# Optimization experiments

Measured on AMD Instinct MI355X. Metric: run time of the kernel, lower is better.

## Reference

```python
import jax, jax.numpy as jnp
import numpy as np

INV_SQRT2 = 0.7071067811865476  # Haar (db1) lowpass on a length-1 zero-padded signal: cA = x/sqrt(2)


def setup_inputs() -> dict:
    key = jax.random.key(0)
    k = jax.random.split(key, 6)
    batch, node, dim = 4, 512, 64
    x = jax.random.normal(k[0], (batch, node, dim), dtype=jnp.float32)
    w0 = jax.random.normal(k[1], (1, 1), dtype=jnp.float32)   # linear[0].weight (always index 0 in source)
    b0 = jax.random.normal(k[2], (1,), dtype=jnp.float32)     # linear[0].bias
    wa = jax.random.normal(k[3], (dim,), dtype=jnp.float32)   # stacked attn_fc[i].weight (each 1x1)
    ba = jax.random.normal(k[4], (dim,), dtype=jnp.float32)   # stacked attn_fc[i].bias
    adj = jax.random.randint(k[5], (node, node), 0, 2, dtype=jnp.int32)
    return {"x": x, "w0": w0, "b0": b0, "wa": wa, "ba": ba, "adj": adj}


def reference(x, w0, b0, wa, ba, adj):
    # x: (b, n, d). Per-channel wavelet feature: softplus(linear0(cA)), cA = x/sqrt(2).
    feat = jax.nn.softplus(x * (INV_SQRT2 * w0[0, 0]) + b0[0])          # (b, n, d)
    scores = feat * wa + ba                                              # (b, n, d): attn_fc[i] per channel
    mask = adj > 0                                                       # (n, n)
    # attn_matrix[b,i,j,d] = scores[b,j,d] * mask[i,j], then masked-fill -1e9 where mask==0
    logits = scores[:, None, :, :] * mask[None, :, :, None].astype(scores.dtype)
    logits = jnp.where(mask[None, :, :, None], logits, jnp.float32(-1e9))
    attn = jax.nn.softmax(logits, axis=2)                                # softmax over j (neighbors)
    out = jnp.einsum('bijd,bjd->bid', attn, feat)                        # (b, n, d)
    return out
```

## Files before the change

kernel.cpp:

```cpp
#include <hip/hip_runtime.h>

#define NODE 512
#define DIM 64
#define BATCH 4

typedef __attribute__((ext_vector_type(8))) short bf16x8;
typedef __attribute__((ext_vector_type(4))) float f32x4;

__device__ __forceinline__ unsigned short f2bf(float f) {
    unsigned int u = __float_as_uint(f);
    u += 0x7FFF + ((u >> 16) & 1);
    return (unsigned short)(u >> 16);
}

__global__ __launch_bounds__(256) void k_fused(const float* __restrict__ x,
                                               const float* __restrict__ w0,
                                               const float* __restrict__ b0,
                                               const float* __restrict__ wa,
                                               const float* __restrict__ ba,
                                               const int* __restrict__ adj,
                                               float* __restrict__ out) {
    const int blk = blockIdx.x;
    const int dt = blk & 3;
    const int it = (blk >> 2) & 31;
    const int b  = blk >> 7;
    const int lane = threadIdx.x & 63;
    const int w    = threadIdx.x >> 6;
    const int fr = lane & 15;
    const int kg = lane >> 4;
    const int i0 = it * 16;
    const int d  = dt * 16 + fr;

    const float c   = 0.7071067811865476f * w0[0];
    const float bb  = b0[0];
    const float wad = wa[d], bad = ba[d];

    const int k0 = w * 128 + kg * 8;
    const int*   pAdj = adj + (i0 + fr) * NODE + k0;
    const float* px   = x + (size_t)b * NODE * DIM + d;

    f32x4 accD = {0.f, 0.f, 0.f, 0.f};
    f32x4 accN = {0.f, 0.f, 0.f, 0.f};

    #pragma unroll
    for (int m = 0; m < 4; ++m) {
        const int jb = k0 + m * 32;
        int4 a0 = *(const int4*)(pAdj + m * 32);
        int4 a1 = *(const int4*)(pAdj + m * 32 + 4);
        union { bf16x8 v; unsigned short s[8]; } A, BD, BN;
        A.s[0] = a0.x ? 0x3F80 : 0;  A.s[1] = a0.y ? 0x3F80 : 0;
        A.s[2] = a0.z ? 0x3F80 : 0;  A.s[3] = a0.w ? 0x3F80 : 0;
        A.s[4] = a1.x ? 0x3F80 : 0;  A.s[5] = a1.y ? 0x3F80 : 0;
        A.s[6] = a1.z ? 0x3F80 : 0;  A.s[7] = a1.w ? 0x3F80 : 0;
        #pragma unroll
        for (int t = 0; t < 8; ++t) {
            float xx = px[(size_t)(jb + t) * DIM];
            float z  = fmaf(xx, c, bb);
            float f  = fmaxf(z, 0.f) + __logf(1.f + __expf(-fabsf(z)));
            float e  = __expf(fmaf(f, wad, bad));
            BD.s[t] = f2bf(e);
            BN.s[t] = f2bf(e * f);
        }
        accD = __builtin_amdgcn_mfma_f32_16x16x32_bf16(A.v, BD.v, accD, 0, 0, 0);
        accN = __builtin_amdgcn_mfma_f32_16x16x32_bf16(A.v, BN.v, accN, 0, 0, 0);
    }

    __shared__ f32x4 red[2][4][64];
    red[0][w][lane] = accD;
    red[1][w][lane] = accN;
    __syncthreads();

    if (w == 0) {
        f32x4 D = red[0][0][lane] + red[0][1][lane] + red[0][2][lane] + red[0][3][lane];
        f32x4 N = red[1][0][lane] + red[1][1][lane] + red[1][2][lane] + red[1][3][lane];
        #pragma unroll
        for (int r = 0; r < 4; ++r) {
            float dd = D[r], nn = N[r];
            float o = (dd != 0.f) ? nn / dd : 0.f;
            out[((b * NODE) + i0 + kg * 4 + r) * DIM + dt * 16 + fr] = o;
        }
    }
}

extern "C" void kernel_launch(void* const* d_in, const int* in_sizes, int n_in,
                              void* d_out, int out_size, void* d_ws, size_t ws_size,
                              hipStream_t stream) {
    const float* x  = (const float*)d_in[0];
    const float* w0 = (const float*)d_in[1];
    const float* b0 = (const float*)d_in[2];
    const float* wa = (const float*)d_in[3];
    const float* ba = (const float*)d_in[4];
    const int*  adj = (const int*)d_in[5];
    float* out = (float*)d_out;

    k_fused<<<dim3(BATCH * 32 * 4), dim3(256), 0, stream>>>(
        x, w0, b0, wa, ba, adj, out);
}
```

Before: 10.56 us.

## Precompute softplus/exp features into LDS and share across two row tiles

Each block now computes the per-neighbor transcendental features (e and e*f in bf16) for all 512 nodes and its 16 channels once, using coalesced float4 loads, and stores them in shared memory. Eight waves then run the MFMA masked sums for two 16-row tiles that read B operands from LDS. Previously every wave recomputed these features per row tile with strided scalar loads. The cost is a larger block, about 33KB of LDS and an extra barrier, and the grid shrinks from 512 to 256 blocks.

Result: faster. 10.32 us (-2.2%).

```diff
diff --git a/kernel.cpp b/kernel.cpp
--- a/kernel.cpp
+++ b/kernel.cpp
@@ -7,77 +7,97 @@
 typedef __attribute__((ext_vector_type(8))) short bf16x8;
 typedef __attribute__((ext_vector_type(4))) float f32x4;
 
+#define LSTRIDE 520
+
 __device__ __forceinline__ unsigned short f2bf(float f) {
     unsigned int u = __float_as_uint(f);
     u += 0x7FFF + ((u >> 16) & 1);
     return (unsigned short)(u >> 16);
 }
 
-__global__ __launch_bounds__(256) void k_fused(const float* __restrict__ x,
-                                               const float* __restrict__ w0,
-                                               const float* __restrict__ b0,
-                                               const float* __restrict__ wa,
-                                               const float* __restrict__ ba,
-                                               const int* __restrict__ adj,
-                                               float* __restrict__ out) {
+__global__ __launch_bounds__(512) void k_fused2(const float* __restrict__ x,
+                                                const float* __restrict__ w0,
+                                                const float* __restrict__ b0,
+                                                const float* __restrict__ wa,
+                                                const float* __restrict__ ba,
+                                                const int* __restrict__ adj,
+                                                float* __restrict__ out) {
+    __shared__ unsigned short Ep[16][LSTRIDE];
+    __shared__ unsigned short Wp[16][LSTRIDE];
+    __shared__ f32x4 red[2][4][2][64];
+
     const int blk = blockIdx.x;
-    const int dt = blk & 3;
-    const int it = (blk >> 2) & 31;
-    const int b  = blk >> 7;
-    const int lane = threadIdx.x & 63;
-    const int w    = threadIdx.x >> 6;
+    const int dt  = blk & 3;
+    const int itg = (blk >> 2) & 15;
+    const int b   = blk >> 6;
+    const int tid = threadIdx.x;
+    const int i0  = itg * 32;
+    const int d0  = dt * 16;
+
+    {
+        const float c  = 0.7071067811865476f * w0[0];
+        const float bb = b0[0];
+        #pragma unroll
+        for (int iter = 0; iter < 4; ++iter) {
+            const int task = iter * 512 + tid;
+            const int dg = task & 3;
+            const int j  = task >> 2;
+            const float4 xx = *(const float4*)(x + ((size_t)(b * NODE + j) * DIM) + d0 + dg * 4);
+            #pragma unroll
+            for (int i = 0; i < 4; ++i) {
+                const int dl = dg * 4 + i;
+                const float xv = (i == 0) ? xx.x : (i == 1) ? xx.y : (i == 2) ? xx.z : xx.w;
+                float z = fmaf(xv, c, bb);
+                float f = fmaxf(z, 0.f) + __logf(1.f + __expf(-fabsf(z)));
+                float e = __expf(fmaf(f, wa[d0 + dl], ba[d0 + dl]));
+                Ep[dl][j] = f2bf(e);
+                Wp[dl][j] = f2bf(e * f);
+            }
+        }
+    }
+    __syncthreads();
+
+    const int lane = tid & 63;
+    const int w    = tid >> 6;
+    const int itl  = w & 1;
+    const int kq   = w >> 1;
     const int fr = lane & 15;
     const int kg = lane >> 4;
-    const int i0 = it * 16;
-    const int d  = dt * 16 + fr;
 
-    const float c   = 0.7071067811865476f * w0[0];
-    const float bb  = b0[0];
-    const float wad = wa[d], bad = ba[d];
-
-    const int k0 = w * 128 + kg * 8;
-    const int*   pAdj = adj + (i0 + fr) * NODE + k0;
-    const float* px   = x + (size_t)b * NODE * DIM + d;
+    const int* pAdj = adj + (i0 + itl * 16 + fr) * NODE + kq * 128 + kg * 8;
+    const int jb0 = kq * 128 + kg * 8;
 
     f32x4 accD = {0.f, 0.f, 0.f, 0.f};
     f32x4 accN = {0.f, 0.f, 0.f, 0.f};
-
     #pragma unroll
     for (int m = 0; m < 4; ++m) {
-        const int jb = k0 + m * 32;
         int4 a0 = *(const int4*)(pAdj + m * 32);
         int4 a1 = *(const int4*)(pAdj + m * 32 + 4);
-        union { bf16x8 v; unsigned short s[8]; } A, BD, BN;
+        union { bf16x8 v; unsigned short s[8]; } A;
         A.s[0] = a0.x ? 0x3F80 : 0;  A.s[1] = a0.y ? 0x3F80 : 0;
         A.s[2] = a0.z ? 0x3F80 : 0;  A.s[3] = a0.w ? 0x3F80 : 0;
         A.s[4] = a1.x ? 0x3F80 : 0;  A.s[5] = a1.y ? 0x3F80 : 0;
         A.s[6] = a1.z ? 0x3F80 : 0;  A.s[7] = a1.w ? 0x3F80 : 0;
-        #pragma unroll
-        for (int t = 0; t < 8; ++t) {
-            float xx = px[(size_t)(jb + t) * DIM];
-            float z  = fmaf(xx, c, bb);
-            float f  = fmaxf(z, 0.f) + __logf(1.f + __expf(-fabsf(z)));
-            float e  = __expf(fmaf(f, wad, bad));
-            BD.s[t] = f2bf(e);
-            BN.s[t] = f2bf(e * f);
-        }
-        accD = __builtin_amdgcn_mfma_f32_16x16x32_bf16(A.v, BD.v, accD, 0, 0, 0);
-        accN = __builtin_amdgcn_mfma_f32_16x16x32_bf16(A.v, BN.v, accN, 0, 0, 0);
+        const int jb = jb0 + m * 32;
+        bf16x8 BD = *(const bf16x8*)&Ep[fr][jb];
+        bf16x8 BN = *(const bf16x8*)&Wp[fr][jb];
+        accD = __builtin_amdgcn_mfma_f32_16x16x32_bf16(A.v, BD, accD, 0, 0, 0);
+        accN = __builtin_amdgcn_mfma_f32_16x16x32_bf16(A.v, BN, accN, 0, 0, 0);
     }
 
-    __shared__ f32x4 red[2][4][64];
-    red[0][w][lane] = accD;
-    red[1][w][lane] = accN;
+    red[itl][kq][0][lane] = accD;
+    red[itl][kq][1][lane] = accN;
     __syncthreads();
 
-    if (w == 0) {
-        f32x4 D = red[0][0][lane] + red[0][1][lane] + red[0][2][lane] + red[0][3][lane];
-        f32x4 N = red[1][0][lane] + red[1][1][lane] + red[1][2][lane] + red[1][3][lane];
+    if (w < 2) {
+        const int t = w;
+        f32x4 D = red[t][0][0][lane] + red[t][1][0][lane] + red[t][2][0][lane] + red[t][3][0][lane];
+        f32x4 N = red[t][0][1][lane] + red[t][1][1][lane] + red[t][2][1][lane] + red[t][3][1][lane];
         #pragma unroll
         for (int r = 0; r < 4; ++r) {
             float dd = D[r], nn = N[r];
             float o = (dd != 0.f) ? nn / dd : 0.f;
-            out[((b * NODE) + i0 + kg * 4 + r) * DIM + dt * 16 + fr] = o;
+            out[((b * NODE) + i0 + t * 16 + kg * 4 + r) * DIM + d0 + fr] = o;
         }
     }
 }
@@ -93,6 +113,5 @@
     const int*  adj = (const int*)d_in[5];
     float* out = (float*)d_out;
 
-    k_fused<<<dim3(BATCH * 32 * 4), dim3(256), 0, stream>>>(
-        x, w0, b0, wa, ba, adj, out);
+    k_fused2<<<dim3(256), dim3(512), 0, stream>>>(x, w0, b0, wa, ba, adj, out);
 }
```
